# Kernel tuning notes

Hardware: AMD Instinct MI355X
Metric: run time of the kernel (lower is better)

The kernel has to match this reference:

```python
import jax, jax.numpy as jnp
import numpy as np

KEEP_RATIO = 0.5
B, H, W = 8, 1024, 1024


def setup_inputs() -> dict:
    key = jax.random.key(0)
    k1, k2, k3 = jax.random.split(key, 3)
    logits = jax.random.normal(k1, (B, 1, H, W), dtype=jnp.float32)
    targets = jax.random.randint(k2, (B, 1, H, W), 0, 2, dtype=jnp.int32)
    tissue_mask = jax.random.randint(k3, (B, 1, H, W), 0, 2, dtype=jnp.int32)
    return {"logits": logits, "targets": targets, "tissue_mask": tissue_mask}


def reference(logits, targets, tissue_mask):
    b = logits.shape[0]
    x = logits.reshape(b, -1)                       # (B, N)
    t = targets.reshape(b, -1).astype(x.dtype)      # {0,1}
    m = tissue_mask.reshape(b, -1).astype(x.dtype)  # {0,1}
    n = x.shape[1]

    # stable binary_cross_entropy_with_logits, reduction='none'
    bce = jnp.maximum(x, 0.0) - x * t + jnp.log1p(jnp.exp(-jnp.abs(x)))
    loss = bce * m                                  # masked per-pixel loss

    pos = t * m                                     # positives inside tissue
    neg = (1.0 - t) * m                             # negatives inside tissue
    n_pos = jnp.sum(pos, axis=1)                    # (B,)
    n_neg = jnp.sum(neg, axis=1)

    k_all = max(1, int(n * KEEP_RATIO))             # static python int
    # kept count per row: all positives + top-(k_all - n_pos) negatives (clamped)
    k_keep = n_pos + jnp.minimum(jnp.maximum(k_all - n_pos, 0.0), n_neg)  # (B,)

    BIG = jnp.asarray(1e30, x.dtype)
    # sort key: positives always first, then negatives by loss, then non-tissue
    sort_key = jnp.where(pos > 0, BIG, jnp.where(neg > 0, loss, -BIG))
    order = jnp.argsort(-sort_key, axis=1)          # descending
    sorted_loss = jnp.take_along_axis(loss, order, axis=1)

    ranks = jnp.arange(n, dtype=x.dtype)
    keep = (ranks[None, :] < k_keep[:, None]).astype(x.dtype)
    per_sample = jnp.sum(sorted_loss * keep, axis=1) / jnp.maximum(k_keep, 1.0)
    # fallback when no tissue pixels at all: torch keeps index 0 (loss there is 0)
    per_sample = jnp.where(k_keep > 0, per_sample, loss[:, 0])
    return jnp.mean(per_sample)
```

## Files before the change

### kernel.cpp

```cpp
#include <hip/hip_runtime.h>
#include <cstdint>
#include <cstddef>

#define N_PIX   1048576
#define B_ROWS  8
#define K_ALL   524288
#define WG_PER_ROW 256
#define ITERS   4
#define NBINS   1024
#define FXSHIFT 11
#define CSHIFT  42
#define SUMMASK ((1ull << CSHIFT) - 1ull)
#define FPSCALE 262144.0f


__global__ __launch_bounds__(256) void k_pass1(
    const float4* __restrict__ lg, const int4* __restrict__ tg, const int4* __restrict__ mk,
    unsigned long long* __restrict__ hist,
    unsigned* __restrict__ partNpos, double* __restrict__ partSpos, float* __restrict__ out)
{
    __shared__ unsigned long long hq[NBINS];
    __shared__ unsigned swp[4];
    __shared__ double   sws[4];
    const int tid = threadIdx.x;

    const int r = blockIdx.x >> 8;
    const size_t base = (size_t)blockIdx.x * (ITERS * 256) + tid;

    float4 x[ITERS]; int4 t[ITERS]; int4 m[ITERS];
    #pragma unroll
    for (int i = 0; i < ITERS; ++i) {
        x[i] = lg[base + (size_t)i * 256];
        t[i] = tg[base + (size_t)i * 256];
        m[i] = mk[base + (size_t)i * 256];
    }
    __builtin_amdgcn_sched_barrier(0);

    for (int b = tid; b < NBINS; b += 256) hq[b] = 0ull;
    if (blockIdx.x == 0 && tid == 0) *out = 0.f;
    __syncthreads();

    unsigned npos = 0; float spos = 0.f;

    auto proc = [&](float xx, int tt, int mm) {
        float ax = fabsf(xx);
        float e = __expf(-ax);
        float l = __logf(1.f + e);
        float bce = fmaxf(xx, 0.f) - xx * (float)tt + l;
        if (mm) {
            if (tt) { npos++; spos += bce; }
            else {
                unsigned fx = (unsigned)__float2uint_rn(bce * FPSCALE);
                unsigned bin = fx >> FXSHIFT;
                if (bin >= NBINS) bin = NBINS - 1;
                atomicAdd(&hq[bin], (1ull << CSHIFT) | (unsigned long long)fx);
            }
        }
    };

    #pragma unroll
    for (int i = 0; i < ITERS; ++i) {
        proc(x[i].x, t[i].x, m[i].x);
        proc(x[i].y, t[i].y, m[i].y);
        proc(x[i].z, t[i].z, m[i].z);
        proc(x[i].w, t[i].w, m[i].w);
    }

    for (int o = 32; o; o >>= 1) {
        npos += __shfl_down(npos, o);
        spos += __shfl_down(spos, o);
    }
    if ((tid & 63) == 0) { swp[tid >> 6] = npos; sws[tid >> 6] = (double)spos; }
    __syncthreads();
    if (tid == 0) {
        partNpos[blockIdx.x] = swp[0] + swp[1] + swp[2] + swp[3];
        partSpos[blockIdx.x] = sws[0] + sws[1] + sws[2] + sws[3];
    }

    unsigned long long* gh = hist + (size_t)r * NBINS;
    for (int b = tid; b < NBINS; b += 256) {
        unsigned long long v = hq[b];
        if (v) atomicAdd(&gh[b], v);
    }
}

__global__ __launch_bounds__(256) void k_final(
    const unsigned long long* __restrict__ hist,
    const unsigned* __restrict__ partNpos, const double* __restrict__ partSpos,
    float* __restrict__ out)
{
    __shared__ unsigned sc[2][256];
    __shared__ double   sd[2][256];
    __shared__ unsigned swp[4];
    __shared__ double   sws[4];
    __shared__ int rT; __shared__ unsigned rcntgt; __shared__ double rsumgt;

    const int r = blockIdx.x, tid = threadIdx.x;
    const unsigned long long* gh = hist + (size_t)r * NBINS;
    const double inv = 1.0 / (double)FPSCALE;

    {
        unsigned np = partNpos[r * 256 + tid];
        double   sp = partSpos[r * 256 + tid];
        for (int o = 32; o; o >>= 1) { np += __shfl_down(np, o); sp += __shfl_down(sp, o); }
        if ((tid & 63) == 0) { swp[tid >> 6] = np; sws[tid >> 6] = sp; }
    }
    __syncthreads();
    const unsigned npos = swp[0] + swp[1] + swp[2] + swp[3];
    const double sumPos = sws[0] + sws[1] + sws[2] + sws[3];
    __syncthreads();

    const int per = NBINS / 256;
    const int b0 = NBINS - 1 - tid * per;
    unsigned lc[4]; double lsum[4];
    unsigned pc = 0; double ps = 0.0;
    #pragma unroll
    for (int i = 0; i < per; ++i) {
        unsigned long long v = gh[b0 - i];
        lc[i] = (unsigned)(v >> CSHIFT);
        lsum[i] = (double)(v & SUMMASK) * inv;
        pc += lc[i]; ps += lsum[i];
    }

    int pp = 0;
    sc[0][tid] = pc; sd[0][tid] = ps;
    __syncthreads();
    for (int ofs = 1; ofs < 256; ofs <<= 1) {
        unsigned c = sc[pp][tid]; double s = sd[pp][tid];
        if (tid >= ofs) { c += sc[pp][tid - ofs]; s += sd[pp][tid - ofs]; }
        sc[pp ^ 1][tid] = c; sd[pp ^ 1][tid] = s;
        pp ^= 1;
        __syncthreads();
    }
    const unsigned nneg   = sc[pp][255];
    const double   sumNeg = sd[pp][255];

    long kl = (long)K_ALL - (long)npos;
    if (kl < 0) kl = 0;
    if (kl > (long)nneg) kl = (long)nneg;
    const unsigned Kneg = (unsigned)kl;

    double sum_sel = 0.0;
    if (Kneg >= nneg) {
        sum_sel = sumNeg;
    } else if (Kneg > 0) {
        unsigned inc = sc[pp][tid];
        unsigned exc = inc - pc;
        double   exs = sd[pp][tid] - ps;
        if (exc < Kneg && Kneg <= inc) {
            unsigned cum = exc; double csum = exs;
            #pragma unroll
            for (int i = 0; i < per; ++i) {
                if (cum + lc[i] >= Kneg) { rT = b0 - i; rcntgt = cum; rsumgt = csum; break; }
                cum += lc[i]; csum += lsum[i];
            }
        }
        __syncthreads();
        if (tid == 0) {
            const int T1 = rT;
            unsigned long long v = gh[T1];
            const unsigned cntT1 = (unsigned)(v >> CSHIFT);
            const double   sumT1 = (double)(v & SUMMASK) * inv;
            const unsigned Kp = Kneg - rcntgt;
            const double lo = (double)T1 * (1.0 / 128.0);
            const double hi = (double)(T1 + 1) * (1.0 / 128.0);
            const double w = hi - lo;
            const double avg = sumT1 / (double)cntT1;
            const double topmean = avg + 0.5 * w * (1.0 - (double)Kp / (double)cntT1);
            sum_sel = rsumgt + (double)Kp * topmean;
        }
    }

    if (tid == 0) {
        unsigned long long kk = (unsigned long long)npos + (unsigned long long)Kneg;
        double per_s = 0.0;
        if (kk > 0) per_s = (sumPos + sum_sel) / (double)kk;
        atomicAdd(out, (float)(per_s / (double)B_ROWS));
    }
}

extern "C" void kernel_launch(void* const* d_in, const int* in_sizes, int n_in,
                              void* d_out, int out_size, void* d_ws, size_t ws_size,
                              hipStream_t stream)
{
    const float* logits = (const float*)d_in[0];
    const int*   targets = (const int*)d_in[1];
    const int*   tissue = (const int*)d_in[2];

    const int NBLK = B_ROWS * WG_PER_ROW;
    char* ws = (char*)d_ws;
    size_t off = 0;
    unsigned long long* hist = (unsigned long long*)(ws + off);
    off += (size_t)B_ROWS * NBINS * 8;
    size_t zero_size = off;
    unsigned* partNpos = (unsigned*)(ws + off); off += (size_t)NBLK * 4;
    double*   partSpos = (double*)(ws + off);   off += (size_t)NBLK * 8;

    hipMemsetAsync(ws, 0, zero_size, stream);

    k_pass1<<<NBLK, 256, 0, stream>>>(
        (const float4*)logits, (const int4*)targets, (const int4*)tissue,
        hist, partNpos, partSpos, (float*)d_out);
    k_final<<<B_ROWS, 256, 0, stream>>>(hist, partNpos, partSpos, (float*)d_out);
}
```

Baseline: 125.9 us.

## Replicate per-row global histograms to spread atomic contention, zero LDS before loads

Each row's global histogram is split into 8 copies, and each workgroup adds its local histogram into the copy picked by blockIdx mod 8. This spreads out the global 64-bit atomics that 256 workgroups per row would otherwise send to the same 1024 bins. The final kernel sums the copies and keeps the threshold bin's count and sum in shared memory, so it no longer rereads that bin. LDS zeroing also moves ahead of the global loads. The cost is a memset 8x larger and extra reads in the final kernel.

Result: no change. 123.5 us (-1.8%).

```diff
diff --git a/kernel.cpp b/kernel.cpp
--- a/kernel.cpp
+++ b/kernel.cpp
@@ -9,6 +9,7 @@
 #define ITERS   4
 #define NBINS   1024
 #define FXSHIFT 11
+#define NCOPY   8
 #define CSHIFT  42
 #define SUMMASK ((1ull << CSHIFT) - 1ull)
 #define FPSCALE 262144.0f
@@ -24,6 +25,11 @@
     __shared__ double   sws[4];
     const int tid = threadIdx.x;
 
+    for (int b = tid; b < NBINS; b += 256) hq[b] = 0ull;
+    if (blockIdx.x == 0 && tid == 0) *out = 0.f;
+    __syncthreads();
+    __builtin_amdgcn_sched_barrier(0);
+
     const int r = blockIdx.x >> 8;
     const size_t base = (size_t)blockIdx.x * (ITERS * 256) + tid;
 
@@ -35,10 +41,6 @@
         m[i] = mk[base + (size_t)i * 256];
     }
     __builtin_amdgcn_sched_barrier(0);
-
-    for (int b = tid; b < NBINS; b += 256) hq[b] = 0ull;
-    if (blockIdx.x == 0 && tid == 0) *out = 0.f;
-    __syncthreads();
 
     unsigned npos = 0; float spos = 0.f;
 
@@ -77,7 +79,7 @@
         partSpos[blockIdx.x] = sws[0] + sws[1] + sws[2] + sws[3];
     }
 
-    unsigned long long* gh = hist + (size_t)r * NBINS;
+    unsigned long long* gh = hist + ((size_t)r * NCOPY + (blockIdx.x & (NCOPY - 1))) * NBINS;
     for (int b = tid; b < NBINS; b += 256) {
         unsigned long long v = hq[b];
         if (v) atomicAdd(&gh[b], v);
@@ -93,10 +95,11 @@
     __shared__ double   sd[2][256];
     __shared__ unsigned swp[4];
     __shared__ double   sws[4];
-    __shared__ int rT; __shared__ unsigned rcntgt; __shared__ double rsumgt;
+    __shared__ int rT; __shared__ unsigned rcntgt, rcnt1;
+    __shared__ double rsumgt, rsum1;
 
     const int r = blockIdx.x, tid = threadIdx.x;
-    const unsigned long long* gh = hist + (size_t)r * NBINS;
+    const unsigned long long* gh = hist + (size_t)r * NCOPY * NBINS;
     const double inv = 1.0 / (double)FPSCALE;
 
     {
@@ -116,7 +119,9 @@
     unsigned pc = 0; double ps = 0.0;
     #pragma unroll
     for (int i = 0; i < per; ++i) {
-        unsigned long long v = gh[b0 - i];
+        unsigned long long v = 0ull;
+        #pragma unroll
+        for (int c = 0; c < NCOPY; ++c) v += gh[(size_t)c * NBINS + (b0 - i)];
         lc[i] = (unsigned)(v >> CSHIFT);
         lsum[i] = (double)(v & SUMMASK) * inv;
         pc += lc[i]; ps += lsum[i];
@@ -151,23 +156,25 @@
             unsigned cum = exc; double csum = exs;
             #pragma unroll
             for (int i = 0; i < per; ++i) {
-                if (cum + lc[i] >= Kneg) { rT = b0 - i; rcntgt = cum; rsumgt = csum; break; }
+                if (cum + lc[i] >= Kneg) {
+                    rT = b0 - i; rcntgt = cum; rsumgt = csum;
+                    rcnt1 = lc[i]; rsum1 = lsum[i];
+                    break;
+                }
                 cum += lc[i]; csum += lsum[i];
             }
         }
         __syncthreads();
         if (tid == 0) {
             const int T1 = rT;
-            unsigned long long v = gh[T1];
-            const unsigned cntT1 = (unsigned)(v >> CSHIFT);
-            const double   sumT1 = (double)(v & SUMMASK) * inv;
+            const unsigned cntT1 = rcnt1;
+            const double   sumT1 = rsum1;
             const unsigned Kp = Kneg - rcntgt;
-            const double lo = (double)T1 * (1.0 / 128.0);
-            const double hi = (double)(T1 + 1) * (1.0 / 128.0);
-            const double w = hi - lo;
+            const double w = 1.0 / 128.0;
             const double avg = sumT1 / (double)cntT1;
             const double topmean = avg + 0.5 * w * (1.0 - (double)Kp / (double)cntT1);
             sum_sel = rsumgt + (double)Kp * topmean;
+            (void)T1;
         }
     }
 
@@ -191,7 +198,7 @@
     char* ws = (char*)d_ws;
     size_t off = 0;
     unsigned long long* hist = (unsigned long long*)(ws + off);
-    off += (size_t)B_ROWS * NBINS * 8;
+    off += (size_t)B_ROWS * NCOPY * NBINS * 8;
     size_t zero_size = off;
     unsigned* partNpos = (unsigned*)(ws + off); off += (size_t)NBLK * 4;
     double*   partSpos = (double*)(ws + off);   off += (size_t)NBLK * 8;
```
